# Performance work log

Hardware: AMD Instinct MI355X
Metric: run time of the kernel (lower is better)

Reference implementation:

```python
import jax, jax.numpy as jnp
import numpy as np

T, H, E, F = 2048, 1024, 32, 512   # tokens, hidden, routed experts, moe intermediate
K, NG, TG = 8, 8, 4                # top_k, n_group, topk_group
FS = 1024                          # shared-expert intermediate = n_shared(2) * F
SCALE = 2.5                        # routed_scaling_factor


def _silu_and_mul(gu):
    g, u = jnp.split(gu, 2, axis=-1)
    return jax.nn.silu(g) * u


def _route(x, gate_w, bias):
    # DeepSeek-V3 noaux_tc grouped top-k with correction bias (sigmoid scores)
    logits = x @ gate_w.T                                   # [T,E]
    scores = jax.nn.sigmoid(logits.astype(jnp.float32))
    sc = scores + bias[None, :]                             # biased scores, selection only
    n_tok = sc.shape[0]
    grp = sc.reshape(n_tok, NG, E // NG)
    top2, _ = jax.lax.top_k(grp, 2)
    group_scores = top2.sum(-1)                             # [T,NG]
    _, gidx = jax.lax.top_k(group_scores, TG)
    gmask = jnp.zeros((n_tok, NG), scores.dtype).at[jnp.arange(n_tok)[:, None], gidx].set(1.0)
    emask = jnp.repeat(gmask, E // NG, axis=1)              # [T,E]
    masked = jnp.where(emask > 0, sc, -jnp.inf)
    _, topk_idx = jax.lax.top_k(masked, K)                  # [T,K]
    w = jnp.take_along_axis(scores, topk_idx, axis=1)       # unbiased scores as weights
    w = w / (w.sum(-1, keepdims=True) + 1e-20)              # renormalize (norm_topk_prob)
    return w, topk_idx


def _forward(x, gate_w, corr_bias, w_gate_up, w_down, shared_gate_up, shared_down):
    w, idx = _route(x, gate_w, corr_bias)
    # dense grouped-GEMM reference: every expert on every token, sparse combine
    gu = jnp.einsum('th,egh->teg', x, w_gate_up)            # [T,E,2F]
    h = _silu_and_mul(gu)                                   # [T,E,F]
    y = jnp.einsum('tef,ehf->teh', h, w_down)               # [T,E,H]
    n_tok = x.shape[0]
    combine = jnp.zeros((n_tok, E), x.dtype).at[jnp.arange(n_tok)[:, None], idx].add(w.astype(x.dtype))
    routed = jnp.einsum('te,teh->th', combine, y) * SCALE
    shared = _silu_and_mul(x @ shared_gate_up.T) @ shared_down.T
    return routed + shared


def setup_inputs() -> dict:
    key = jax.random.key(0)
    ks = jax.random.split(key, 7)
    return {
        "hidden_states": jax.random.normal(ks[0], (T, H), jnp.float32),
        "gate_w": jax.random.normal(ks[1], (E, H), jnp.float32) * 0.02,
        "corr_bias": jax.random.normal(ks[2], (E,), jnp.float32) * 0.01,
        "w_gate_up": jax.random.normal(ks[3], (E, 2 * F, H), jnp.float32) * 0.02,
        "w_down": jax.random.normal(ks[4], (E, H, F), jnp.float32) * 0.02,
        "shared_gate_up": jax.random.normal(ks[5], (2 * FS, H), jnp.float32) * 0.02,
        "shared_down": jax.random.normal(ks[6], (H, FS), jnp.float32) * 0.02,
        "num_global_tokens": T,
        "max_num_tokens_per_gpu": T,
    }


def reference(hidden_states, gate_w, corr_bias, w_gate_up, w_down, shared_gate_up, shared_down, num_global_tokens, max_num_tokens_per_gpu):
    return _forward(hidden_states, gate_w, corr_bias, w_gate_up, w_down, shared_gate_up, shared_down)
```

## Files before the change

kernel.cpp:

```cpp
#include <hip/hip_runtime.h>
#include <hip/hip_bf16.h>

#define T_TOK 2048
#define H_DIM 1024
#define E_EXP 32
#define F_DIM 512
#define FS_DIM 1024
#define K_TOP 8
#define NGRP 8
#define TGRP 4
#define GSZ (E_EXP / NGRP)
#define RSCALE 2.5f
#define CAP 2048

typedef short  short8 __attribute__((ext_vector_type(8)));
typedef __bf16 bf16x4 __attribute__((ext_vector_type(4)));
typedef float  f32x4  __attribute__((ext_vector_type(4)));

__global__ void cvt_all(const float* __restrict__ s0, __bf16* __restrict__ d0, int n0,
                        const float* __restrict__ s1, __bf16* __restrict__ d1, int n1,
                        const float* __restrict__ s2, __bf16* __restrict__ d2, int n2,
                        const float* __restrict__ s3, __bf16* __restrict__ d3, int n3) {
  const int ntot = n0 + n1 + n2 + n3;
  int gid = blockIdx.x * blockDim.x + threadIdx.x;
  const int stride = gridDim.x * blockDim.x;
  for (; gid < ntot; gid += stride) {
    int i = gid;
    const float* src; __bf16* dst;
    if (i < n0) { src = s0; dst = d0; }
    else { i -= n0;
      if (i < n1) { src = s1; dst = d1; }
      else { i -= n1;
        if (i < n2) { src = s2; dst = d2; }
        else { i -= n2; src = s3; dst = d3; }
      }
    }
    const float4 v = reinterpret_cast<const float4*>(src)[i];
    bf16x4 o;
    o[0] = (__bf16)v.x; o[1] = (__bf16)v.y; o[2] = (__bf16)v.z; o[3] = (__bf16)v.w;
    reinterpret_cast<bf16x4*>(dst)[i] = o;
  }
}

__global__ __launch_bounds__(64) void route_kernel(
    const float* __restrict__ x, const float* __restrict__ gw,
    const float* __restrict__ bias, int* __restrict__ tk_idx,
    float* __restrict__ tk_w, __bf16* __restrict__ xb) {
  const int t = blockIdx.x;
  const int lane = threadIdx.x;
  float xr[16];
#pragma unroll
  for (int i = 0; i < 16; i++) xr[i] = x[t * H_DIM + i * 64 + lane];
#pragma unroll
  for (int i = 0; i < 16; i++) xb[t * H_DIM + i * 64 + lane] = (__bf16)xr[i];
  float sc[E_EXP];
#pragma unroll
  for (int e = 0; e < E_EXP; e++) {
    const float* w = gw + e * H_DIM;
    float s = 0.f;
#pragma unroll
    for (int i = 0; i < 16; i++) s += xr[i] * w[i * 64 + lane];
#pragma unroll
    for (int off = 32; off > 0; off >>= 1) s += __shfl_xor(s, off);
    sc[e] = 1.f / (1.f + expf(-s));
  }
  if (lane == 0) {
    float b[E_EXP];
    for (int e = 0; e < E_EXP; e++) b[e] = sc[e] + bias[e];
    float gs[NGRP];
    for (int g = 0; g < NGRP; g++) {
      float m1 = -1e30f, m2 = -1e30f;
      for (int j = 0; j < GSZ; j++) {
        float v = b[g * GSZ + j];
        if (v > m1) { m2 = m1; m1 = v; } else if (v > m2) { m2 = v; }
      }
      gs[g] = m1 + m2;
    }
    unsigned gmask = 0;
    for (int it = 0; it < TGRP; it++) {
      float best = -1e30f; int bi = 0;
      for (int g = 0; g < NGRP; g++)
        if (!((gmask >> g) & 1) && gs[g] > best) { best = gs[g]; bi = g; }
      gmask |= 1u << bi;
    }
    unsigned emask = 0; float wsum = 0.f;
    int idx8[K_TOP];
    for (int it = 0; it < K_TOP; it++) {
      float best = -1e30f; int bi = 0;
      for (int e = 0; e < E_EXP; e++) {
        if (!((gmask >> (e / GSZ)) & 1)) continue;
        if ((emask >> e) & 1) continue;
        if (b[e] > best) { best = b[e]; bi = e; }
      }
      emask |= 1u << bi;
      idx8[it] = bi;
      wsum += sc[bi];
    }
    const float inv = 1.f / (wsum + 1e-20f);
    for (int k = 0; k < K_TOP; k++) {
      tk_idx[t * K_TOP + k] = idx8[k];
      tk_w[t * K_TOP + k] = sc[idx8[k]] * inv;
    }
  }
}

__global__ void scatter_kernel(const int* __restrict__ tk_idx, int* __restrict__ counts,
                               int* __restrict__ recs) {
  const int i = blockIdx.x * blockDim.x + threadIdx.x;
  if (i >= T_TOK * K_TOP) return;
  const int e = tk_idx[i];
  const int pos = atomicAdd(&counts[e], 1);
  recs[e * CAP + pos] = i;
}

#define BM 128
#define BN 128
#define BK 64

__device__ __forceinline__ void gload_lds16(const void* g, void* l) {
  __builtin_amdgcn_global_load_lds(
      (__attribute__((address_space(1))) const void*)g,
      (__attribute__((address_space(3))) void*)l, 16, 0, 0);
}

template <int PHASE>
__global__ __launch_bounds__(256) void gemm_fused(
    const __bf16* __restrict__ Ar, const __bf16* __restrict__ As_,
    const __bf16* __restrict__ Br, const __bf16* __restrict__ Bs_,
    void* __restrict__ OutR, void* __restrict__ OutS,
    const int* __restrict__ recs, const int* __restrict__ counts,
    const float* __restrict__ tk_w) {

  const int z = blockIdx.z;
  const bool routed = (z < E_EXP);
  const int e = z;
  const int m0 = blockIdx.y * BM;
  const int bx = blockIdx.x;

  int count = T_TOK, off_e = 0;
  if (routed) {
    count = counts[e];
    for (int i = 0; i < E_EXP; i++) off_e += (i < e) ? counts[i] : 0;
    if (m0 >= count) return;
  }
  const int K = (PHASE == 0) ? H_DIM : (routed ? F_DIM : FS_DIM);

  const int tid = threadIdx.x, wid = tid >> 6, lane = tid & 63;

  __shared__ __align__(16) __bf16 Atile[BM * BK];
  __shared__ __align__(16) __bf16 Btile[BN * BK];

  const int colk = (lane & 7) * 8;
  const __bf16* aptr[4];
  const __bf16* bptr[4];
#pragma unroll
  for (int i = 0; i < 4; i++) {
    const int row = wid * 32 + i * 8 + (lane >> 3);
    int r = m0 + row; if (r > count - 1) r = count - 1;
    if (PHASE == 0) {
      if (routed) {
        const int rec = recs[e * CAP + r];
        aptr[i] = Ar + (size_t)(rec >> 3) * H_DIM + colk;
      } else {
        aptr[i] = As_ + (size_t)r * H_DIM + colk;
      }
    } else {
      if (routed) aptr[i] = Ar + (size_t)(off_e + r) * F_DIM + colk;
      else        aptr[i] = As_ + (size_t)r * FS_DIM + colk;
    }
    if (PHASE == 0) {
      if (routed) {
        const int brow = (row < 64) ? (bx * 64 + row) : (F_DIM + bx * 64 + row - 64);
        bptr[i] = Br + (size_t)e * 2 * F_DIM * H_DIM + (size_t)brow * H_DIM + colk;
      } else {
        const int s = z - E_EXP;
        const int fglob = s * 512 + bx * 64 + (row & 63);
        const int brow = (row < 64) ? fglob : (FS_DIM + fglob);
        bptr[i] = Bs_ + (size_t)brow * H_DIM + colk;
      }
    } else {
      if (routed) {
        const int brow = bx * BN + row;
        bptr[i] = Br + (size_t)e * H_DIM * F_DIM + (size_t)brow * F_DIM + colk;
      } else {
        const int brow = bx * BN + row;
        bptr[i] = Bs_ + (size_t)brow * FS_DIM + colk;
      }
    }
  }

  f32x4 acc[2][8];
#pragma unroll
  for (int a = 0; a < 2; a++)
#pragma unroll
    for (int b = 0; b < 8; b++) acc[a][b] = f32x4{0.f, 0.f, 0.f, 0.f};

  const int lr = lane & 15, lh = lane >> 4;

  for (int k0 = 0; k0 < K; k0 += BK) {
#pragma unroll
    for (int i = 0; i < 4; i++)
      gload_lds16(aptr[i] + k0, (char*)Atile + (wid * 4 + i) * 1024);
#pragma unroll
    for (int i = 0; i < 4; i++)
      gload_lds16(bptr[i] + k0, (char*)Btile + (wid * 4 + i) * 1024);
    __syncthreads();
#pragma unroll
    for (int kk = 0; kk < 2; kk++) {
      short8 af[2], bfr[8];
#pragma unroll
      for (int fm = 0; fm < 2; fm++)
        af[fm] = *reinterpret_cast<const short8*>(&Atile[(wid * 32 + fm * 16 + lr) * BK + kk * 32 + lh * 8]);
#pragma unroll
      for (int fn = 0; fn < 8; fn++)
        bfr[fn] = *reinterpret_cast<const short8*>(&Btile[(fn * 16 + lr) * BK + kk * 32 + lh * 8]);
#pragma unroll
      for (int fn = 0; fn < 8; fn++)
#pragma unroll
        for (int fm = 0; fm < 2; fm++)
          acc[fm][fn] = __builtin_amdgcn_mfma_f32_16x16x32_bf16(af[fm], bfr[fn], acc[fm][fn], 0, 0, 0);
    }
    __syncthreads();
  }

  if (PHASE == 0) {
#pragma unroll
    for (int fm = 0; fm < 2; fm++)
#pragma unroll
      for (int j = 0; j < 4; j++) {
        const int row = wid * 32 + fm * 16 + lh * 4 + j;
        if (m0 + row < count) {
#pragma unroll
          for (int fn = 0; fn < 4; fn++) {
            const float g = acc[fm][fn][j], u = acc[fm][fn + 4][j];
            const float hv = g / (1.f + expf(-g)) * u;
            if (routed) {
              const int f = bx * 64 + fn * 16 + lr;
              ((__bf16*)OutR)[(size_t)(off_e + m0 + row) * F_DIM + f] = (__bf16)hv;
            } else {
              const int s = z - E_EXP;
              const int f = s * 512 + bx * 64 + fn * 16 + lr;
              ((__bf16*)OutS)[(size_t)(m0 + row) * FS_DIM + f] = (__bf16)hv;
            }
          }
        }
      }
  } else {
#pragma unroll
    for (int fm = 0; fm < 2; fm++)
#pragma unroll
      for (int j = 0; j < 4; j++) {
        const int row = wid * 32 + fm * 16 + lh * 4 + j;
        if (m0 + row < count) {
          if (routed) {
            const int rec = recs[e * CAP + m0 + row];
            const float w = tk_w[rec];
            const size_t base = (size_t)rec * H_DIM + bx * BN;
#pragma unroll
            for (int fn = 0; fn < 8; fn++)
              ((float*)OutR)[base + fn * 16 + lr] = acc[fm][fn][j] * w;
          } else {
#pragma unroll
            for (int fn = 0; fn < 8; fn++)
              ((float*)OutS)[(size_t)(m0 + row) * H_DIM + bx * BN + fn * 16 + lr] = acc[fm][fn][j];
          }
        }
      }
  }
}

__global__ void combine_kernel(const float* __restrict__ y_slot, float* __restrict__ out) {
  const int gid = blockIdx.x * blockDim.x + threadIdx.x;
  const int t = gid >> 8;
  const int c0 = (gid & 255) * 4;
  float4 s = {0.f, 0.f, 0.f, 0.f};
#pragma unroll
  for (int k = 0; k < K_TOP; k++) {
    const float4 v = *reinterpret_cast<const float4*>(&y_slot[((size_t)t * K_TOP + k) * H_DIM + c0]);
    s.x += v.x; s.y += v.y; s.z += v.z; s.w += v.w;
  }
  float4 o = *reinterpret_cast<float4*>(&out[(size_t)t * H_DIM + c0]);
  o.x += RSCALE * s.x; o.y += RSCALE * s.y; o.z += RSCALE * s.z; o.w += RSCALE * s.w;
  *reinterpret_cast<float4*>(&out[(size_t)t * H_DIM + c0]) = o;
}

extern "C" void kernel_launch(void* const* d_in, const int* in_sizes, int n_in,
                              void* d_out, int out_size, void* d_ws, size_t ws_size,
                              hipStream_t stream) {
  const float* x    = (const float*)d_in[0];
  const float* gw   = (const float*)d_in[1];
  const float* bias = (const float*)d_in[2];
  const float* wgu  = (const float*)d_in[3];
  const float* wd   = (const float*)d_in[4];
  const float* sgu  = (const float*)d_in[5];
  const float* sd   = (const float*)d_in[6];

  char* ws = (char*)d_ws;
  size_t o = 0;
  auto alloc = [&](size_t bytes) {
    char* p = ws + o;
    o += (bytes + 255) & ~(size_t)255;
    return (void*)p;
  };
  __bf16* xb     = (__bf16*)alloc((size_t)T_TOK * H_DIM * 2);
  __bf16* wgub   = (__bf16*)alloc((size_t)E_EXP * 2 * F_DIM * H_DIM * 2);
  __bf16* wdb    = (__bf16*)alloc((size_t)E_EXP * H_DIM * F_DIM * 2);
  __bf16* sgub   = (__bf16*)alloc((size_t)2 * FS_DIM * H_DIM * 2);
  __bf16* sdb    = (__bf16*)alloc((size_t)H_DIM * FS_DIM * 2);
  __bf16* h_buf  = (__bf16*)alloc((size_t)T_TOK * K_TOP * F_DIM * 2);
  float*  y_slot = (float*) alloc((size_t)T_TOK * K_TOP * H_DIM * 4);
  __bf16* hs     = (__bf16*)alloc((size_t)T_TOK * FS_DIM * 2);
  int*   tk_idx  = (int*)  alloc((size_t)T_TOK * K_TOP * 4);
  float* tk_w    = (float*)alloc((size_t)T_TOK * K_TOP * 4);
  int*   counts  = (int*)  alloc((size_t)E_EXP * 4);
  int*   recs    = (int*)  alloc((size_t)E_EXP * CAP * 4);
  if (o > ws_size) return;

  cvt_all<<<2048, 256, 0, stream>>>(
      wgu, wgub, E_EXP * 2 * F_DIM * H_DIM / 4,
      wd,  wdb,  E_EXP * H_DIM * F_DIM / 4,
      sgu, sgub, 2 * FS_DIM * H_DIM / 4,
      sd,  sdb,  H_DIM * FS_DIM / 4);

  route_kernel<<<T_TOK, 64, 0, stream>>>(x, gw, bias, tk_idx, tk_w, xb);

  hipMemsetAsync(counts, 0, E_EXP * 4, stream);
  scatter_kernel<<<(T_TOK * K_TOP + 255) / 256, 256, 0, stream>>>(tk_idx, counts, recs);

  gemm_fused<0><<<dim3(F_DIM / 64, T_TOK / BM, E_EXP + 2), 256, 0, stream>>>(
      xb, xb, wgub, sgub, h_buf, hs, recs, counts, tk_w);

  gemm_fused<1><<<dim3(H_DIM / BN, T_TOK / BM, E_EXP + 1), 256, 0, stream>>>(
      h_buf, hs, wdb, sdb, y_slot, d_out, recs, counts, tk_w);

  combine_kernel<<<T_TOK * H_DIM / 4 / 256, 256, 0, stream>>>(y_slot, (float*)d_out);
}
```

Measured before the change: 310.9 us.

## Use 256x256 tiles with double-buffered swizzled LDS in grouped MoE GEMMs

Replaces the 128x128, 256-thread GEMM with a 256x256 tile computed by 512 threads in a 2x4 wave grid. The K loop is double-buffered with async global-to-LDS loads, using explicit vmcnt waits and barriers so the next tile loads while MFMAs run. LDS columns are XOR-swizzled to cut bank conflicts. The aim is more reuse per tile and hidden load latency. The costs are heavier per-thread register use and more padded waste on experts with few tokens, since routed experts average about 512 tokens, which is only two M tiles.

```diff
diff --git a/kernel.cpp b/kernel.cpp
--- a/kernel.cpp
+++ b/kernel.cpp
@@ -113,8 +113,6 @@
   recs[e * CAP + pos] = i;
 }
 
-#define BM 128
-#define BN 128
 #define BK 64
 
 __device__ __forceinline__ void gload_lds16(const void* g, void* l) {
@@ -124,7 +122,7 @@
 }
 
 template <int PHASE>
-__global__ __launch_bounds__(256) void gemm_fused(
+__global__ __launch_bounds__(512, 2) void gemm256(
     const __bf16* __restrict__ Ar, const __bf16* __restrict__ As_,
     const __bf16* __restrict__ Br, const __bf16* __restrict__ Bs_,
     void* __restrict__ OutR, void* __restrict__ OutS,
@@ -133,24 +131,26 @@
 
   const int z = blockIdx.z;
   const bool routed = (z < E_EXP);
-  const int e = z;
-  const int m0 = blockIdx.y * BM;
+  const int m0 = blockIdx.y * 256;
   const int bx = blockIdx.x;
 
   int count = T_TOK, off_e = 0;
   if (routed) {
-    count = counts[e];
-    for (int i = 0; i < E_EXP; i++) off_e += (i < e) ? counts[i] : 0;
+    count = counts[z];
+    for (int i = 0; i < E_EXP; i++) off_e += (i < z) ? counts[i] : 0;
     if (m0 >= count) return;
   }
   const int K = (PHASE == 0) ? H_DIM : (routed ? F_DIM : FS_DIM);
+  const int NT = K / BK;
 
   const int tid = threadIdx.x, wid = tid >> 6, lane = tid & 63;
-
-  __shared__ __align__(16) __bf16 Atile[BM * BK];
-  __shared__ __align__(16) __bf16 Btile[BN * BK];
-
-  const int colk = (lane & 7) * 8;
+  const int wr = wid >> 2, wc = wid & 3;
+  const int lr = lane & 15, lh = lane >> 4;
+
+  __shared__ __align__(16) __bf16 As[2][256 * BK];
+  __shared__ __align__(16) __bf16 Bs[2][256 * BK];
+
+  const int colk = (((lane & 7) ^ (lane >> 3)) * 8);
   const __bf16* aptr[4];
   const __bf16* bptr[4];
 #pragma unroll
@@ -159,7 +159,7 @@
     int r = m0 + row; if (r > count - 1) r = count - 1;
     if (PHASE == 0) {
       if (routed) {
-        const int rec = recs[e * CAP + r];
+        const int rec = recs[z * CAP + r];
         aptr[i] = Ar + (size_t)(rec >> 3) * H_DIM + colk;
       } else {
         aptr[i] = As_ + (size_t)r * H_DIM + colk;
@@ -169,77 +169,86 @@
       else        aptr[i] = As_ + (size_t)r * FS_DIM + colk;
     }
     if (PHASE == 0) {
+      const int sub = row & 63, wcb = row >> 6;
       if (routed) {
-        const int brow = (row < 64) ? (bx * 64 + row) : (F_DIM + bx * 64 + row - 64);
-        bptr[i] = Br + (size_t)e * 2 * F_DIM * H_DIM + (size_t)brow * H_DIM + colk;
+        const int f = bx * 128 + wcb * 32 + (sub & 31);
+        const int brow = (sub < 32) ? f : (F_DIM + f);
+        bptr[i] = Br + (size_t)z * 2 * F_DIM * H_DIM + (size_t)brow * H_DIM + colk;
       } else {
-        const int s = z - E_EXP;
-        const int fglob = s * 512 + bx * 64 + (row & 63);
-        const int brow = (row < 64) ? fglob : (FS_DIM + fglob);
+        const int f = (z - E_EXP) * 512 + bx * 128 + wcb * 32 + (sub & 31);
+        const int brow = (sub < 32) ? f : (FS_DIM + f);
         bptr[i] = Bs_ + (size_t)brow * H_DIM + colk;
       }
     } else {
-      if (routed) {
-        const int brow = bx * BN + row;
-        bptr[i] = Br + (size_t)e * H_DIM * F_DIM + (size_t)brow * F_DIM + colk;
-      } else {
-        const int brow = bx * BN + row;
-        bptr[i] = Bs_ + (size_t)brow * FS_DIM + colk;
-      }
-    }
-  }
-
-  f32x4 acc[2][8];
-#pragma unroll
-  for (int a = 0; a < 2; a++)
-#pragma unroll
-    for (int b = 0; b < 8; b++) acc[a][b] = f32x4{0.f, 0.f, 0.f, 0.f};
-
-  const int lr = lane & 15, lh = lane >> 4;
-
-  for (int k0 = 0; k0 < K; k0 += BK) {
-#pragma unroll
-    for (int i = 0; i < 4; i++)
-      gload_lds16(aptr[i] + k0, (char*)Atile + (wid * 4 + i) * 1024);
-#pragma unroll
-    for (int i = 0; i < 4; i++)
-      gload_lds16(bptr[i] + k0, (char*)Btile + (wid * 4 + i) * 1024);
-    __syncthreads();
+      if (routed) bptr[i] = Br + (size_t)z * H_DIM * F_DIM + (size_t)(bx * 256 + row) * F_DIM + colk;
+      else        bptr[i] = Bs_ + (size_t)(bx * 256 + row) * FS_DIM + colk;
+    }
+  }
+
+  auto STAGE = [&](int buf, int k0) {
+#pragma unroll
+    for (int i = 0; i < 4; i++) {
+      gload_lds16(aptr[i] + k0, (char*)&As[buf][0] + (wid * 32 + i * 8) * 128);
+      gload_lds16(bptr[i] + k0, (char*)&Bs[buf][0] + (wid * 32 + i * 8) * 128);
+    }
+  };
+
+  f32x4 acc[8][4];
+#pragma unroll
+  for (int a = 0; a < 8; a++)
+#pragma unroll
+    for (int b = 0; b < 4; b++) acc[a][b] = f32x4{0.f, 0.f, 0.f, 0.f};
+
+  STAGE(0, 0);
+  STAGE(1, BK);
+
+  int cur = 0;
+  for (int t = 0; t < NT; ++t) {
+    if (t + 1 < NT) asm volatile("s_waitcnt vmcnt(8)" ::: "memory");
+    else            asm volatile("s_waitcnt vmcnt(0)" ::: "memory");
+    __builtin_amdgcn_s_barrier();
 #pragma unroll
     for (int kk = 0; kk < 2; kk++) {
-      short8 af[2], bfr[8];
-#pragma unroll
-      for (int fm = 0; fm < 2; fm++)
-        af[fm] = *reinterpret_cast<const short8*>(&Atile[(wid * 32 + fm * 16 + lr) * BK + kk * 32 + lh * 8]);
-#pragma unroll
-      for (int fn = 0; fn < 8; fn++)
-        bfr[fn] = *reinterpret_cast<const short8*>(&Btile[(fn * 16 + lr) * BK + kk * 32 + lh * 8]);
-#pragma unroll
-      for (int fn = 0; fn < 8; fn++)
-#pragma unroll
-        for (int fm = 0; fm < 2; fm++)
+      short8 af[8], bfr[4];
+#pragma unroll
+      for (int fm = 0; fm < 8; fm++) {
+        const int row = wr * 128 + fm * 16 + lr;
+        af[fm] = *reinterpret_cast<const short8*>(
+            &As[cur][row * 64 + (((kk * 4 + lh) ^ (lr & 7)) * 8)]);
+      }
+#pragma unroll
+      for (int fn = 0; fn < 4; fn++) {
+        const int row = wc * 64 + fn * 16 + lr;
+        bfr[fn] = *reinterpret_cast<const short8*>(
+            &Bs[cur][row * 64 + (((kk * 4 + lh) ^ (lr & 7)) * 8)]);
+      }
+#pragma unroll
+      for (int fn = 0; fn < 4; fn++)
+#pragma unroll
+        for (int fm = 0; fm < 8; fm++)
           acc[fm][fn] = __builtin_amdgcn_mfma_f32_16x16x32_bf16(af[fm], bfr[fn], acc[fm][fn], 0, 0, 0);
     }
-    __syncthreads();
+    __builtin_amdgcn_s_barrier();
+    if (t + 2 < NT) STAGE(cur, (t + 2) * BK);
+    cur ^= 1;
   }
 
   if (PHASE == 0) {
 #pragma unroll
-    for (int fm = 0; fm < 2; fm++)
+    for (int fm = 0; fm < 8; fm++)
 #pragma unroll
       for (int j = 0; j < 4; j++) {
-        const int row = wid * 32 + fm * 16 + lh * 4 + j;
+        const int row = wr * 128 + fm * 16 + lh * 4 + j;
         if (m0 + row < count) {
 #pragma unroll
-          for (int fn = 0; fn < 4; fn++) {
-            const float g = acc[fm][fn][j], u = acc[fm][fn + 4][j];
+          for (int fn = 0; fn < 2; fn++) {
+            const float g = acc[fm][fn][j], u = acc[fm][fn + 2][j];
             const float hv = g / (1.f + expf(-g)) * u;
             if (routed) {
-              const int f = bx * 64 + fn * 16 + lr;
+              const int f = bx * 128 + wc * 32 + fn * 16 + lr;
               ((__bf16*)OutR)[(size_t)(off_e + m0 + row) * F_DIM + f] = (__bf16)hv;
             } else {
-              const int s = z - E_EXP;
-              const int f = s * 512 + bx * 64 + fn * 16 + lr;
+              const int f = (z - E_EXP) * 512 + bx * 128 + wc * 32 + fn * 16 + lr;
               ((__bf16*)OutS)[(size_t)(m0 + row) * FS_DIM + f] = (__bf16)hv;
             }
           }
@@ -247,22 +256,22 @@
       }
   } else {
 #pragma unroll
-    for (int fm = 0; fm < 2; fm++)
+    for (int fm = 0; fm < 8; fm++)
 #pragma unroll
       for (int j = 0; j < 4; j++) {
-        const int row = wid * 32 + fm * 16 + lh * 4 + j;
+        const int row = wr * 128 + fm * 16 + lh * 4 + j;
         if (m0 + row < count) {
           if (routed) {
-            const int rec = recs[e * CAP + m0 + row];
+            const int rec = recs[z * CAP + m0 + row];
             const float w = tk_w[rec];
-            const size_t base = (size_t)rec * H_DIM + bx * BN;
-#pragma unroll
-            for (int fn = 0; fn < 8; fn++)
+            const size_t base = (size_t)rec * H_DIM + bx * 256 + wc * 64;
+#pragma unroll
+            for (int fn = 0; fn < 4; fn++)
               ((float*)OutR)[base + fn * 16 + lr] = acc[fm][fn][j] * w;
           } else {
 #pragma unroll
-            for (int fn = 0; fn < 8; fn++)
-              ((float*)OutS)[(size_t)(m0 + row) * H_DIM + bx * BN + fn * 16 + lr] = acc[fm][fn][j];
+            for (int fn = 0; fn < 4; fn++)
+              ((float*)OutS)[(size_t)(m0 + row) * H_DIM + bx * 256 + wc * 64 + fn * 16 + lr] = acc[fm][fn][j];
           }
         }
       }
@@ -327,10 +336,10 @@
   hipMemsetAsync(counts, 0, E_EXP * 4, stream);
   scatter_kernel<<<(T_TOK * K_TOP + 255) / 256, 256, 0, stream>>>(tk_idx, counts, recs);
 
-  gemm_fused<0><<<dim3(F_DIM / 64, T_TOK / BM, E_EXP + 2), 256, 0, stream>>>(
+  gemm256<0><<<dim3(4, 8, E_EXP + 2), 512, 0, stream>>>(
       xb, xb, wgub, sgub, h_buf, hs, recs, counts, tk_w);
 
-  gemm_fused<1><<<dim3(H_DIM / BN, T_TOK / BM, E_EXP + 1), 256, 0, stream>>>(
+  gemm256<1><<<dim3(4, 8, E_EXP + 1), 512, 0, stream>>>(
       h_buf, hs, wdb, sdb, y_slot, d_out, recs, counts, tk_w);
 
   combine_kernel<<<T_TOK * H_DIM / 4 / 256, 256, 0, stream>>>(y_slot, (float*)d_out);
```

After: 436.1 us. +40.3%, slower.

## Double-buffer LDS tiles to overlap global loads with MFMA compute

Applied to the files above, without the earlier changes.

Adds a second LDS buffer for the A and B tiles in the grouped GEMM kernel. The next K-tile is issued with direct global-to-LDS loads before the MFMAs on the current tile run, and there is one wait plus barrier per iteration instead of two syncthreads. This is meant to hide global memory latency behind matrix math, at the cost of twice the shared memory per block, which may lower occupancy.

```diff
diff --git a/kernel.cpp b/kernel.cpp
--- a/kernel.cpp
+++ b/kernel.cpp
@@ -144,11 +144,12 @@
     if (m0 >= count) return;
   }
   const int K = (PHASE == 0) ? H_DIM : (routed ? F_DIM : FS_DIM);
+  const int NT = K / BK;
 
   const int tid = threadIdx.x, wid = tid >> 6, lane = tid & 63;
 
-  __shared__ __align__(16) __bf16 Atile[BM * BK];
-  __shared__ __align__(16) __bf16 Btile[BN * BK];
+  __shared__ __align__(16) __bf16 Atile[2][BM * BK];
+  __shared__ __align__(16) __bf16 Btile[2][BN * BK];
 
   const int colk = (lane & 7) * 8;
   const __bf16* aptr[4];
@@ -189,6 +190,15 @@
     }
   }
 
+  auto STAGE = [&](int buf, int k0) {
+#pragma unroll
+    for (int i = 0; i < 4; i++)
+      gload_lds16(aptr[i] + k0, (char*)Atile[buf] + (wid * 4 + i) * 1024);
+#pragma unroll
+    for (int i = 0; i < 4; i++)
+      gload_lds16(bptr[i] + k0, (char*)Btile[buf] + (wid * 4 + i) * 1024);
+  };
+
   f32x4 acc[2][8];
 #pragma unroll
   for (int a = 0; a < 2; a++)
@@ -197,30 +207,36 @@
 
   const int lr = lane & 15, lh = lane >> 4;
 
-  for (int k0 = 0; k0 < K; k0 += BK) {
-#pragma unroll
-    for (int i = 0; i < 4; i++)
-      gload_lds16(aptr[i] + k0, (char*)Atile + (wid * 4 + i) * 1024);
-#pragma unroll
-    for (int i = 0; i < 4; i++)
-      gload_lds16(bptr[i] + k0, (char*)Btile + (wid * 4 + i) * 1024);
-    __syncthreads();
+  STAGE(0, 0);
+  asm volatile("s_waitcnt vmcnt(0)" ::: "memory");
+  __builtin_amdgcn_s_barrier();
+
+  int cur = 0;
+  for (int t = 0; t < NT; ++t) {
+    if (t + 1 < NT) {
+      STAGE(cur ^ 1, (t + 1) * BK);
+      __builtin_amdgcn_sched_barrier(0);
+    }
 #pragma unroll
     for (int kk = 0; kk < 2; kk++) {
       short8 af[2], bfr[8];
 #pragma unroll
       for (int fm = 0; fm < 2; fm++)
-        af[fm] = *reinterpret_cast<const short8*>(&Atile[(wid * 32 + fm * 16 + lr) * BK + kk * 32 + lh * 8]);
+        af[fm] = *reinterpret_cast<const short8*>(&Atile[cur][(wid * 32 + fm * 16 + lr) * BK + kk * 32 + lh * 8]);
 #pragma unroll
       for (int fn = 0; fn < 8; fn++)
-        bfr[fn] = *reinterpret_cast<const short8*>(&Btile[(fn * 16 + lr) * BK + kk * 32 + lh * 8]);
+        bfr[fn] = *reinterpret_cast<const short8*>(&Btile[cur][(fn * 16 + lr) * BK + kk * 32 + lh * 8]);
 #pragma unroll
       for (int fn = 0; fn < 8; fn++)
 #pragma unroll
         for (int fm = 0; fm < 2; fm++)
           acc[fm][fn] = __builtin_amdgcn_mfma_f32_16x16x32_bf16(af[fm], bfr[fn], acc[fm][fn], 0, 0, 0);
     }
-    __syncthreads();
+    if (t + 1 < NT) {
+      asm volatile("s_waitcnt vmcnt(0)" ::: "memory");
+      __builtin_amdgcn_s_barrier();
+      cur ^= 1;
+    }
   }
 
   if (PHASE == 0) {
```

Measured after the change: 322.0 us. +3.6%, slower.

## Overlap weight conversion with routing and gate-up GEMM via extra blocks

Applied to the files above, without the earlier changes.

Merges the routing kernel and the gate/up weight conversion into one prep kernel, with routing handling 4 tokens per 256-thread block and the remaining blocks converting weights. The down-projection weight conversion moves into an extra z-slice of the phase-0 GEMM grid, so it runs alongside the first GEMM instead of in a separate kernel. This is meant to remove a launch and to hide the bandwidth-bound fp32-to-bf16 conversion behind compute. In exchange, the conversion blocks compete with GEMM blocks for CU slots and memory bandwidth.

```diff
diff --git a/kernel.cpp b/kernel.cpp
--- a/kernel.cpp
+++ b/kernel.cpp
@@ -17,89 +17,93 @@
 typedef __bf16 bf16x4 __attribute__((ext_vector_type(4)));
 typedef float  f32x4  __attribute__((ext_vector_type(4)));
 
-__global__ void cvt_all(const float* __restrict__ s0, __bf16* __restrict__ d0, int n0,
-                        const float* __restrict__ s1, __bf16* __restrict__ d1, int n1,
-                        const float* __restrict__ s2, __bf16* __restrict__ d2, int n2,
-                        const float* __restrict__ s3, __bf16* __restrict__ d3, int n3) {
-  const int ntot = n0 + n1 + n2 + n3;
-  int gid = blockIdx.x * blockDim.x + threadIdx.x;
-  const int stride = gridDim.x * blockDim.x;
-  for (; gid < ntot; gid += stride) {
-    int i = gid;
-    const float* src; __bf16* dst;
-    if (i < n0) { src = s0; dst = d0; }
-    else { i -= n0;
-      if (i < n1) { src = s1; dst = d1; }
-      else { i -= n1;
-        if (i < n2) { src = s2; dst = d2; }
-        else { i -= n2; src = s3; dst = d3; }
-      }
-    }
-    const float4 v = reinterpret_cast<const float4*>(src)[i];
-    bf16x4 o;
-    o[0] = (__bf16)v.x; o[1] = (__bf16)v.y; o[2] = (__bf16)v.z; o[3] = (__bf16)v.w;
-    reinterpret_cast<bf16x4*>(dst)[i] = o;
-  }
-}
-
-__global__ __launch_bounds__(64) void route_kernel(
+__device__ __forceinline__ void cvt4_split(const float* __restrict__ s0, __bf16* __restrict__ d0, int n0,
+                                           const float* __restrict__ s1, __bf16* __restrict__ d1, int j) {
+  const float* src = (j < n0) ? s0 : s1;
+  __bf16* dst = (j < n0) ? d0 : d1;
+  const int i = (j < n0) ? j : (j - n0);
+  const float4 v = reinterpret_cast<const float4*>(src)[i];
+  bf16x4 o;
+  o[0] = (__bf16)v.x; o[1] = (__bf16)v.y; o[2] = (__bf16)v.z; o[3] = (__bf16)v.w;
+  reinterpret_cast<bf16x4*>(dst)[i] = o;
+}
+
+#define NROUTE_BLK (T_TOK / 4)
+__global__ __launch_bounds__(256) void prep_kernel(
     const float* __restrict__ x, const float* __restrict__ gw,
     const float* __restrict__ bias, int* __restrict__ tk_idx,
-    float* __restrict__ tk_w, __bf16* __restrict__ xb) {
-  const int t = blockIdx.x;
-  const int lane = threadIdx.x;
-  float xr[16];
-#pragma unroll
-  for (int i = 0; i < 16; i++) xr[i] = x[t * H_DIM + i * 64 + lane];
-#pragma unroll
-  for (int i = 0; i < 16; i++) xb[t * H_DIM + i * 64 + lane] = (__bf16)xr[i];
-  float sc[E_EXP];
-#pragma unroll
-  for (int e = 0; e < E_EXP; e++) {
-    const float* w = gw + e * H_DIM;
-    float s = 0.f;
-#pragma unroll
-    for (int i = 0; i < 16; i++) s += xr[i] * w[i * 64 + lane];
-#pragma unroll
-    for (int off = 32; off > 0; off >>= 1) s += __shfl_xor(s, off);
-    sc[e] = 1.f / (1.f + expf(-s));
-  }
-  if (lane == 0) {
-    float b[E_EXP];
-    for (int e = 0; e < E_EXP; e++) b[e] = sc[e] + bias[e];
-    float gs[NGRP];
-    for (int g = 0; g < NGRP; g++) {
-      float m1 = -1e30f, m2 = -1e30f;
-      for (int j = 0; j < GSZ; j++) {
-        float v = b[g * GSZ + j];
-        if (v > m1) { m2 = m1; m1 = v; } else if (v > m2) { m2 = v; }
-      }
-      gs[g] = m1 + m2;
-    }
-    unsigned gmask = 0;
-    for (int it = 0; it < TGRP; it++) {
-      float best = -1e30f; int bi = 0;
-      for (int g = 0; g < NGRP; g++)
-        if (!((gmask >> g) & 1) && gs[g] > best) { best = gs[g]; bi = g; }
-      gmask |= 1u << bi;
-    }
-    unsigned emask = 0; float wsum = 0.f;
-    int idx8[K_TOP];
-    for (int it = 0; it < K_TOP; it++) {
-      float best = -1e30f; int bi = 0;
-      for (int e = 0; e < E_EXP; e++) {
-        if (!((gmask >> (e / GSZ)) & 1)) continue;
-        if ((emask >> e) & 1) continue;
-        if (b[e] > best) { best = b[e]; bi = e; }
-      }
-      emask |= 1u << bi;
-      idx8[it] = bi;
-      wsum += sc[bi];
-    }
-    const float inv = 1.f / (wsum + 1e-20f);
-    for (int k = 0; k < K_TOP; k++) {
-      tk_idx[t * K_TOP + k] = idx8[k];
-      tk_w[t * K_TOP + k] = sc[idx8[k]] * inv;
+    float* __restrict__ tk_w, __bf16* __restrict__ xb,
+    const float* __restrict__ wgu, __bf16* __restrict__ wgub,
+    const float* __restrict__ sgu, __bf16* __restrict__ sgub) {
+  if (blockIdx.x < NROUTE_BLK) {
+    const int wid = threadIdx.x >> 6, lane = threadIdx.x & 63;
+    const int t = blockIdx.x * 4 + wid;
+    float xr[16];
+#pragma unroll
+    for (int i = 0; i < 16; i++) xr[i] = x[t * H_DIM + i * 64 + lane];
+#pragma unroll
+    for (int i = 0; i < 16; i++) xb[t * H_DIM + i * 64 + lane] = (__bf16)xr[i];
+    float sc[E_EXP];
+#pragma unroll
+    for (int e = 0; e < E_EXP; e++) {
+      const float* w = gw + e * H_DIM;
+      float s = 0.f;
+#pragma unroll
+      for (int i = 0; i < 16; i++) s += xr[i] * w[i * 64 + lane];
+#pragma unroll
+      for (int off = 32; off > 0; off >>= 1) s += __shfl_xor(s, off);
+      sc[e] = 1.f / (1.f + expf(-s));
+    }
+    if (lane == 0) {
+      float b[E_EXP];
+      for (int e = 0; e < E_EXP; e++) b[e] = sc[e] + bias[e];
+      float gs[NGRP];
+      for (int g = 0; g < NGRP; g++) {
+        float m1 = -1e30f, m2 = -1e30f;
+        for (int j = 0; j < GSZ; j++) {
+          float v = b[g * GSZ + j];
+          if (v > m1) { m2 = m1; m1 = v; } else if (v > m2) { m2 = v; }
+        }
+        gs[g] = m1 + m2;
+      }
+      unsigned gmask = 0;
+      for (int it = 0; it < TGRP; it++) {
+        float best = -1e30f; int bi = 0;
+        for (int g = 0; g < NGRP; g++)
+          if (!((gmask >> g) & 1) && gs[g] > best) { best = gs[g]; bi = g; }
+        gmask |= 1u << bi;
+      }
+      unsigned emask = 0; float wsum = 0.f;
+      int idx8[K_TOP];
+      for (int it = 0; it < K_TOP; it++) {
+        float best = -1e30f; int bi = 0;
+        for (int e = 0; e < E_EXP; e++) {
+          if (!((gmask >> (e / GSZ)) & 1)) continue;
+          if ((emask >> e) & 1) continue;
+          if (b[e] > best) { best = b[e]; bi = e; }
+        }
+        emask |= 1u << bi;
+        idx8[it] = bi;
+        wsum += sc[bi];
+      }
+      const float inv = 1.f / (wsum + 1e-20f);
+      for (int k = 0; k < K_TOP; k++) {
+        tk_idx[t * K_TOP + k] = idx8[k];
+        tk_w[t * K_TOP + k] = sc[idx8[k]] * inv;
+      }
+    }
+  } else {
+    const int n0 = E_EXP * 2 * F_DIM * H_DIM / 4;
+    const int n1 = 2 * FS_DIM * H_DIM / 4;
+    const int ntot = n0 + n1;
+    const int nthr = (gridDim.x - NROUTE_BLK) * 256;
+    const int base = (blockIdx.x - NROUTE_BLK) * 256 + threadIdx.x;
+    for (int i = base; i < ntot; i += 4 * nthr) {
+#pragma unroll
+      for (int u = 0; u < 4; u++) {
+        const int j = i + u * nthr;
+        if (j < ntot) cvt4_split(wgu, wgub, n0, sgu, sgub, j);
+      }
     }
   }
 }
@@ -129,9 +133,28 @@
     const __bf16* __restrict__ Br, const __bf16* __restrict__ Bs_,
     void* __restrict__ OutR, void* __restrict__ OutS,
     const int* __restrict__ recs, const int* __restrict__ counts,
-    const float* __restrict__ tk_w) {
+    const float* __restrict__ tk_w,
+    const float* __restrict__ cvt_s0, __bf16* __restrict__ cvt_d0,
+    const float* __restrict__ cvt_s1, __bf16* __restrict__ cvt_d1) {
 
   const int z = blockIdx.z;
+
+  if (PHASE == 0 && z == E_EXP + 2) {
+    const int n0 = E_EXP * H_DIM * F_DIM / 4;
+    const int n1 = H_DIM * FS_DIM / 4;
+    const int ntot = n0 + n1;
+    const int nthr = gridDim.x * gridDim.y * 256;
+    const int base = (blockIdx.y * gridDim.x + blockIdx.x) * 256 + threadIdx.x;
+    for (int i = base; i < ntot; i += 4 * nthr) {
+#pragma unroll
+      for (int u = 0; u < 4; u++) {
+        const int j = i + u * nthr;
+        if (j < ntot) cvt4_split(cvt_s0, cvt_d0, n0, cvt_s1, cvt_d1, j);
+      }
+    }
+    return;
+  }
+
   const bool routed = (z < E_EXP);
   const int e = z;
   const int m0 = blockIdx.y * BM;
@@ -316,22 +339,17 @@
   int*   recs    = (int*)  alloc((size_t)E_EXP * CAP * 4);
   if (o > ws_size) return;
 
-  cvt_all<<<2048, 256, 0, stream>>>(
-      wgu, wgub, E_EXP * 2 * F_DIM * H_DIM / 4,
-      wd,  wdb,  E_EXP * H_DIM * F_DIM / 4,
-      sgu, sgub, 2 * FS_DIM * H_DIM / 4,
-      sd,  sdb,  H_DIM * FS_DIM / 4);
-
-  route_kernel<<<T_TOK, 64, 0, stream>>>(x, gw, bias, tk_idx, tk_w, xb);
-
   hipMemsetAsync(counts, 0, E_EXP * 4, stream);
+  prep_kernel<<<2048, 256, 0, stream>>>(x, gw, bias, tk_idx, tk_w, xb, wgu, wgub, sgu, sgub);
+
   scatter_kernel<<<(T_TOK * K_TOP + 255) / 256, 256, 0, stream>>>(tk_idx, counts, recs);
 
-  gemm_fused<0><<<dim3(F_DIM / 64, T_TOK / BM, E_EXP + 2), 256, 0, stream>>>(
-      xb, xb, wgub, sgub, h_buf, hs, recs, counts, tk_w);
+  gemm_fused<0><<<dim3(F_DIM / 64, T_TOK / BM, E_EXP + 3), 256, 0, stream>>>(
+      xb, xb, wgub, sgub, h_buf, hs, recs, counts, tk_w, wd, wdb, sd, sdb);
 
   gemm_fused<1><<<dim3(H_DIM / BN, T_TOK / BM, E_EXP + 1), 256, 0, stream>>>(
-      h_buf, hs, wdb, sdb, y_slot, d_out, recs, counts, tk_w);
+      h_buf, hs, wdb, sdb, y_slot, d_out, recs, counts, tk_w,
+      (const float*)nullptr, (__bf16*)nullptr, (const float*)nullptr, (__bf16*)nullptr);
 
   combine_kernel<<<T_TOK * H_DIM / 4 / 256, 256, 0, stream>>>(y_slot, (float*)d_out);
 }
```

After: 332.0 us. +6.8%, slower.
